# Kernel optimization log

Hardware: AMD Instinct MI355X
Metric: run time of the kernel (lower is better)

The kernel has to match this reference:

```python
import jax, jax.numpy as jnp
import numpy as np
from jax.ops import segment_sum

EPS = 1e-5
N, E = 100000, 1600000
CIN, H, COUT, ED = 32, 64, 16, 16


def _lin(k, fan_in, fan_out):
    return jax.random.normal(k, (fan_in, fan_out), jnp.float32) / np.sqrt(fan_in)


def setup_inputs() -> dict:
    key = jax.random.key(0)
    ks = jax.random.split(key, 24)
    inp = {
        "x": jax.random.normal(ks[0], (N, CIN), jnp.float32),
        "edge_index": jax.random.randint(ks[1], (2, E), 0, N, jnp.int32),
        "edge_attr": jax.random.normal(ks[2], (E, ED), jnp.float32),
    }
    # layer 1 (SAGEConvWithEdgeAttr: in=CIN -> H)
    inp.update(
        l1_Wl=_lin(ks[3], CIN, H), l1_bl=jnp.zeros((H,), jnp.float32),
        l1_Wr=_lin(ks[4], CIN, H),
        l1_We=_lin(ks[5], ED, H), l1_be=jnp.zeros((H,), jnp.float32),
        l1_Wg=_lin(ks[6], 2 * H, H), l1_bg=jnp.zeros((H,), jnp.float32),
        l1_bng=jnp.ones((H,), jnp.float32), l1_bnb=jnp.zeros((H,), jnp.float32),
    )
    # layer 2 (H -> H)
    inp.update(
        l2_Wl=_lin(ks[7], H, H), l2_bl=jnp.zeros((H,), jnp.float32),
        l2_Wr=_lin(ks[8], H, H),
        l2_We=_lin(ks[9], ED, H), l2_be=jnp.zeros((H,), jnp.float32),
        l2_Wg=_lin(ks[10], 2 * H, H), l2_bg=jnp.zeros((H,), jnp.float32),
        l2_bng=jnp.ones((H,), jnp.float32), l2_bnb=jnp.zeros((H,), jnp.float32),
    )
    # GraphNorms (weight=1, bias=0, mean_scale=1 at init; randomize slightly via ones)
    inp.update(
        gn1_g=jnp.ones((H,), jnp.float32), gn1_b=jnp.zeros((H,), jnp.float32), gn1_a=jnp.ones((H,), jnp.float32),
        gn2_g=jnp.ones((H,), jnp.float32), gn2_b=jnp.zeros((H,), jnp.float32), gn2_a=jnp.ones((H,), jnp.float32),
        lin_W=_lin(ks[11], H, COUT), lin_b=jnp.zeros((COUT,), jnp.float32),
    )
    return inp


def _sage_edge_layer(x, row, col, ea, Wl, bl, Wr, We, be, Wg, bg, bng, bnb):
    n = x.shape[0]
    ea_t = ea @ We + be                                        # [E', H]
    deg = segment_sum(jnp.ones_like(col, dtype=x.dtype), col, num_segments=n)
    agg = segment_sum(x[row], col, num_segments=n) / jnp.maximum(deg, 1.0)[:, None]
    out = agg @ Wl + bl + x @ Wr                               # SAGEConv (mean)
    gate = jax.nn.sigmoid(jnp.concatenate([out[col], ea_t], -1) @ Wg + bg)
    out = out + segment_sum(gate * ea_t, col, num_segments=n)  # edge contributions
    mu = out.mean(0)
    var = ((out - mu) ** 2).mean(0)                            # BatchNorm1d (batch stats)
    out = bng * (out - mu) * jax.lax.rsqrt(var + EPS) + bnb
    return jax.nn.relu(2.0 * out)                              # Identity residual + out, relu


def _graph_norm(x, g, b, a):
    mu = x.mean(0)
    xc = x - a * mu
    var = (xc ** 2).mean(0)
    return g * xc * jax.lax.rsqrt(var + EPS) + b


def reference(x, edge_index, edge_attr,
              l1_Wl, l1_bl, l1_Wr, l1_We, l1_be, l1_Wg, l1_bg, l1_bng, l1_bnb,
              l2_Wl, l2_bl, l2_Wr, l2_We, l2_be, l2_Wg, l2_bg, l2_bng, l2_bnb,
              gn1_g, gn1_b, gn1_a, gn2_g, gn2_b, gn2_a, lin_W, lin_b):
    n = x.shape[0]
    loop = jnp.arange(n, dtype=edge_index.dtype)
    row = jnp.concatenate([edge_index[0], loop])               # add_self_loops
    col = jnp.concatenate([edge_index[1], loop])
    ea = jnp.concatenate([edge_attr, jnp.ones((n, edge_attr.shape[1]), edge_attr.dtype)], 0)
    h = _sage_edge_layer(x, row, col, ea, l1_Wl, l1_bl, l1_Wr, l1_We, l1_be, l1_Wg, l1_bg, l1_bng, l1_bnb)
    h = jax.nn.relu(h)
    h = jax.nn.relu(_graph_norm(h, gn1_g, gn1_b, gn1_a))
    h = _sage_edge_layer(h, row, col, ea, l2_Wl, l2_bl, l2_Wr, l2_We, l2_be, l2_Wg, l2_bg, l2_bng, l2_bnb)
    h = jax.nn.relu(h)
    h = jax.nn.relu(_graph_norm(h, gn2_g, gn2_b, gn2_a))
    return h @ lin_W + lin_b
```

## Files before the change

kernel.cpp:

```cpp
#include <hip/hip_runtime.h>
#include <hip/hip_fp16.h>
#include <math.h>
#include <stdint.h>

#define H 64
#define ED 16
#define CO 16
#define WGRID 2048
#define NWAVES (WGRID * 4)
#define CPART 2048
static constexpr float EPSV = 1e-5f;
static constexpr float LOG2E = 1.44269504f;

typedef _Float16 h2v __attribute__((ext_vector_type(2)));
typedef _Float16 f16x8 __attribute__((ext_vector_type(8)));
typedef float f32x4 __attribute__((ext_vector_type(4)));

__device__ __forceinline__ float sigm2(float z) {
    return __builtin_amdgcn_rcpf(1.0f + __builtin_amdgcn_exp2f(-z));
}

__device__ __forceinline__ h2v as_h2(int x) { union { int i; h2v h; } u; u.i = x; return u.h; }

__device__ __forceinline__ f16x8 as_f16x8(int4 v) { union { int4 i; f16x8 h; } u; u.i = v; return u.h; }

__device__ __forceinline__ int pack2(float a, float b) {
    __half2 h = __floats2half2_rn(a, b);
    return *reinterpret_cast<int*>(&h);
}

__global__ void k_prep(const float* __restrict__ We1, const float* __restrict__ be1, const float* __restrict__ Wg1,
                       const float* __restrict__ We2, const float* __restrict__ be2, const float* __restrict__ Wg2,
                       float* __restrict__ ws) {
    int j = threadIdx.x;
    for (int l = 0; l < 2; ++l) {
        const float* We = l ? We2 : We1;
        const float* be = l ? be2 : be1;
        const float* Wg = l ? Wg2 : Wg1;
        int* wth = (int*)(ws + (l ? 1024 : 0));
        int* wgh = (int*)(ws + (l ? 1536 : 512));
        float* ets = ws + 2048 + l * 192;
        float* vs  = ws + 2112 + l * 192;
        float* dv  = ws + 2176 + l * 192;
        float wt[ED], wg[ED];
        float et = be[j];
        for (int k = 0; k < ED; ++k) { wt[k] = We[k * H + j]; et += wt[k]; }
        ets[j] = et;
        float d = 0.f;
        for (int m = 0; m < H; ++m) d += be[m] * Wg[(H + m) * H + j];
        float vsum = d;
        for (int k = 0; k < ED; ++k) {
            float acc = 0.f;
            for (int m = 0; m < H; ++m) acc += We[k * H + m] * Wg[(H + m) * H + j];
            wg[k] = acc;
            vsum += acc;
        }
        dv[j] = d * LOG2E;
        vs[j] = vsum * LOG2E;
        for (int q = 0; q < 8; ++q) {
            wth[j * 8 + q] = pack2(wt[2 * q], wt[2 * q + 1]);
            wgh[j * 8 + q] = pack2(wg[2 * q] * LOG2E, wg[2 * q + 1] * LOG2E);
        }
    }
    for (int s = 0; s < 8; ++s) ws[2432 + s * 64 + j] = 0.f;
}

__global__ void k_xh(const float* __restrict__ x, __half* __restrict__ xh, int total4) {
    int i = blockIdx.x * blockDim.x + threadIdx.x;
    if (i >= total4) return;
    float4 v = *reinterpret_cast<const float4*>(x + (size_t)i * 4);
    __half2 h0 = __floats2half2_rn(v.x, v.y), h1 = __floats2half2_rn(v.z, v.w);
    uint2 o;
    o.x = *reinterpret_cast<unsigned*>(&h0);
    o.y = *reinterpret_cast<unsigned*>(&h1);
    *reinterpret_cast<uint2*>(xh + (size_t)i * 4) = o;
}

__global__ void k_eah(const float* __restrict__ ea, int4* __restrict__ eah, int E) {
    int e = blockIdx.x * blockDim.x + threadIdx.x;
    if (e >= E) return;
    const float4* src = reinterpret_cast<const float4*>(ea + (size_t)e * ED);
    float4 v0 = src[0], v1 = src[1], v2 = src[2], v3 = src[3];
    int hh[8];
    hh[0] = pack2(v0.x, v0.y); hh[1] = pack2(v0.z, v0.w);
    hh[2] = pack2(v1.x, v1.y); hh[3] = pack2(v1.z, v1.w);
    hh[4] = pack2(v2.x, v2.y); hh[5] = pack2(v2.z, v2.w);
    hh[6] = pack2(v3.x, v3.y); hh[7] = pack2(v3.z, v3.w);
    const int4* o = reinterpret_cast<const int4*>(hh);
    eah[(size_t)e * 2 + 0] = o[0];
    eah[(size_t)e * 2 + 1] = o[1];
}

__global__ void k_count(const int* __restrict__ cols, int* __restrict__ cnt, int E) {
    int e = blockIdx.x * blockDim.x + threadIdx.x;
    if (e < E) atomicAdd(&cnt[cols[e]], 1);
}

__global__ __launch_bounds__(1024) void k_scan1(const int* __restrict__ cnt, int* __restrict__ bs, int N) {
    __shared__ int ls[1024];
    int t = threadIdx.x;
    int i = blockIdx.x * 1024 + t;
    ls[t] = (i < N) ? cnt[i] : 0;
    __syncthreads();
    for (int off = 512; off > 0; off >>= 1) {
        if (t < off) ls[t] += ls[t + off];
        __syncthreads();
    }
    if (t == 0) bs[blockIdx.x] = ls[0];
}

__global__ __launch_bounds__(1024) void k_scan2(int* __restrict__ bs, int SB) {
    __shared__ int ls[1024];
    int t = threadIdx.x;
    int v = (t < SB) ? bs[t] : 0;
    ls[t] = v;
    __syncthreads();
    for (int off = 1; off < 1024; off <<= 1) {
        int x = (t >= off) ? ls[t - off] : 0;
        __syncthreads();
        ls[t] += x;
        __syncthreads();
    }
    if (t < SB) bs[t] = ls[t] - v;
}

__global__ __launch_bounds__(1024) void k_scan3(const int* __restrict__ cnt, const int* __restrict__ bs,
                                                int* __restrict__ rowptr, int N, int E) {
    __shared__ int ls[1024];
    int t = threadIdx.x;
    int i = blockIdx.x * 1024 + t;
    int v = (i < N) ? cnt[i] : 0;
    ls[t] = v;
    __syncthreads();
    for (int off = 1; off < 1024; off <<= 1) {
        int x = (t >= off) ? ls[t - off] : 0;
        __syncthreads();
        ls[t] += x;
        __syncthreads();
    }
    if (i < N) rowptr[i] = bs[blockIdx.x] + ls[t] - v;
    if (i == 0) rowptr[N] = E;
}

__global__ void k_ranges(const int* __restrict__ rowptr, int* __restrict__ ranges, int N, int E, int nw) {
    int w = blockIdx.x * blockDim.x + threadIdx.x;
    if (w > nw) return;
    if (w == nw) { ranges[nw] = N; return; }
    int t0 = (int)((long)E * w / nw);
    int lo = 0, hi = N;
    while (lo < hi) { int mid = (lo + hi) >> 1; if (rowptr[mid] < t0) lo = mid + 1; else hi = mid; }
    ranges[w] = lo;
}

__global__ __launch_bounds__(256) void k_part(const int* __restrict__ rows, const int* __restrict__ cols,
                                              int2* __restrict__ tmp, int* __restrict__ offtab,
                                              int E, int NB, int SH) {
    __shared__ int hist[1025];
    __shared__ int pscan[256];
    __shared__ int2 stage[CPART];
    int tid = threadIdx.x;
    int base = blockIdx.x * CPART;
    int cnt = min(CPART, E - base);
    for (int i = tid; i <= NB; i += 256) hist[i] = 0;
    __syncthreads();
    int myc[8], myr[8];
#pragma unroll
    for (int q = 0; q < 8; ++q) {
        int li = q * 256 + tid;
        if (li < cnt) {
            int e = base + li;
            myc[q] = cols[e];
            myr[q] = rows[e];
            atomicAdd(&hist[myc[q] >> SH], 1);
        } else myc[q] = -1;
    }
    __syncthreads();
    int h[4], s = 0;
    int b0 = tid * 4;
#pragma unroll
    for (int k = 0; k < 4; ++k) { h[k] = (b0 + k < NB) ? hist[b0 + k] : 0; s += h[k]; }
    pscan[tid] = s;
    __syncthreads();
    for (int off = 1; off < 256; off <<= 1) {
        int v = (tid >= off) ? pscan[tid - off] : 0;
        __syncthreads();
        pscan[tid] += v;
        __syncthreads();
    }
    int excl = pscan[tid] - s;
    __syncthreads();
    int run = excl;
#pragma unroll
    for (int k = 0; k < 4; ++k) {
        if (b0 + k < NB) hist[b0 + k] = run;
        run += h[k];
    }
    __syncthreads();
    int* ot = offtab + (size_t)blockIdx.x * (NB + 1);
    for (int i = tid; i < NB; i += 256) ot[i] = hist[i];
    if (tid == 0) ot[NB] = cnt;
    __syncthreads();
    int mask = (1 << SH) - 1;
#pragma unroll
    for (int q = 0; q < 8; ++q) {
        if (myc[q] >= 0) {
            int b = myc[q] >> SH;
            int p = atomicAdd(&hist[b], 1);
            int e = base + q * 256 + tid;
            stage[p] = make_int2(myr[q], (e << SH) | (myc[q] & mask));
        }
    }
    __syncthreads();
    int2* dst = tmp + base;
    for (int i = tid; i < cnt; i += 256) dst[i] = stage[i];
}

__global__ __launch_bounds__(1024) void k_build(const int* __restrict__ rowptr, const int2* __restrict__ tmp,
                                               const int* __restrict__ offtab, const int4* __restrict__ eah,
                                               int* __restrict__ erow, __half* __restrict__ eap,
                                               int N, int NB, int SH, int PB) {
    __shared__ int lcur[1024];
    int tid = threadIdx.x;
    int b = blockIdx.x;
    int NPB = 1 << SH;
    int nodelo = b << SH;
    for (int j = tid; j < NPB; j += 1024) {
        int n = nodelo + j;
        lcur[j] = (n < N) ? rowptr[n] : 0;
    }
    __syncthreads();
    int mask = NPB - 1;
    for (int i = tid; i < PB; i += 1024) {
        const int* ot = offtab + (size_t)i * (NB + 1);
        int j0 = ot[b], j1 = ot[b + 1];
        for (int j = j0; j < j1; ++j) {
            int2 v = tmp[(size_t)i * CPART + j];
            int e = (int)(((unsigned)v.y) >> SH);
            int cl = v.y & mask;
            int p = atomicAdd(&lcur[cl], 1);
            erow[p] = v.x;
            int4 a0 = eah[(size_t)e * 2 + 0];
            int4 a1 = eah[(size_t)e * 2 + 1];
            int4* d = reinterpret_cast<int4*>(eap + (size_t)p * ED);
            d[0] = a0; d[1] = a1;
        }
    }
}

template <int CIN, bool GN>
__global__ __launch_bounds__(256) void k_gather(const __half* __restrict__ x, const int* __restrict__ rowptr,
                         const int* __restrict__ ranges,
                         const int* __restrict__ erow, float* __restrict__ agg,
                         const float* __restrict__ s1, const float* __restrict__ s2,
                         const float* __restrict__ gng, const float* __restrict__ gnb,
                         const float* __restrict__ gna, float Ninv, int N) {
    int lane = threadIdx.x & 63;
    int w = (blockIdx.x * blockDim.x + threadIdx.x) >> 6;
    float A = 1.f, B = 0.f;
    if (GN) {
        float mu = s1[lane] * Ninv, m2 = s2[lane] * Ninv, a = gna[lane];
        float var = m2 - 2.f * a * mu * mu + a * a * mu * mu;
        A = gng[lane] * rsqrtf(var + EPSV);
        B = gnb[lane] - A * a * mu;
    }
    int n0 = ranges[w], n1 = ranges[w + 1];
    for (int n = n0; n < n1; ++n) {
        int s = rowptr[n], te = rowptr[n + 1];
        if (CIN == 64) {
            float raw = __half2float(x[(size_t)n * 64 + lane]);
            float acc = GN ? fmaxf(fmaf(A, raw, B), 0.f) : raw;
            int i = s;
            for (; i + 7 < te; i += 8) {
                int r0 = erow[i],     r1 = erow[i + 1], r2 = erow[i + 2], r3 = erow[i + 3];
                int r4 = erow[i + 4], r5 = erow[i + 5], r6 = erow[i + 6], r7 = erow[i + 7];
                float x0 = __half2float(x[(size_t)r0 * 64 + lane]);
                float x1 = __half2float(x[(size_t)r1 * 64 + lane]);
                float x2 = __half2float(x[(size_t)r2 * 64 + lane]);
                float x3 = __half2float(x[(size_t)r3 * 64 + lane]);
                float x4 = __half2float(x[(size_t)r4 * 64 + lane]);
                float x5 = __half2float(x[(size_t)r5 * 64 + lane]);
                float x6 = __half2float(x[(size_t)r6 * 64 + lane]);
                float x7 = __half2float(x[(size_t)r7 * 64 + lane]);
                if (GN) {
                    x0 = fmaxf(fmaf(A, x0, B), 0.f); x1 = fmaxf(fmaf(A, x1, B), 0.f);
                    x2 = fmaxf(fmaf(A, x2, B), 0.f); x3 = fmaxf(fmaf(A, x3, B), 0.f);
                    x4 = fmaxf(fmaf(A, x4, B), 0.f); x5 = fmaxf(fmaf(A, x5, B), 0.f);
                    x6 = fmaxf(fmaf(A, x6, B), 0.f); x7 = fmaxf(fmaf(A, x7, B), 0.f);
                }
                acc += ((x0 + x1) + (x2 + x3)) + ((x4 + x5) + (x6 + x7));
            }
            for (; i < te; ++i) {
                float xv = __half2float(x[(size_t)erow[i] * 64 + lane]);
                if (GN) xv = fmaxf(fmaf(A, xv, B), 0.f);
                acc += xv;
            }
            agg[(size_t)n * H + lane] = acc;
        } else {
            int c = lane & 31, half = lane >> 5;
            float acc = half ? 0.f : __half2float(x[(size_t)n * 32 + c]);
            int i = s + half;
            for (; i + 6 < te; i += 8) {
                int r0 = erow[i], r1 = erow[i + 2], r2 = erow[i + 4], r3 = erow[i + 6];
                float x0 = __half2float(x[(size_t)r0 * 32 + c]);
                float x1 = __half2float(x[(size_t)r1 * 32 + c]);
                float x2 = __half2float(x[(size_t)r2 * 32 + c]);
                float x3 = __half2float(x[(size_t)r3 * 32 + c]);
                acc += (x0 + x1) + (x2 + x3);
            }
            for (; i < te; i += 2) acc += __half2float(x[(size_t)erow[i] * 32 + c]);
            acc += __shfl_xor(acc, 32);
            if (half == 0) agg[(size_t)n * H + c] = acc;
        }
    }
}

#define MT4A(mq, aval) \
    acc[mq][0] = fmaf(aval, w1.x, acc[mq][0]); acc[mq][1] = fmaf(aval, w1.y, acc[mq][1]); \
    acc[mq][2] = fmaf(aval, w1.z, acc[mq][2]); acc[mq][3] = fmaf(aval, w1.w, acc[mq][3]);
#define MT4X(mq, aval) \
    acc[mq][0] = fmaf(aval, w2.x, acc[mq][0]); acc[mq][1] = fmaf(aval, w2.y, acc[mq][1]); \
    acc[mq][2] = fmaf(aval, w2.z, acc[mq][2]); acc[mq][3] = fmaf(aval, w2.w, acc[mq][3]);

template <int K, bool GN>
__global__ __launch_bounds__(256) void k_gemmfu(
        const float* __restrict__ A,
        const __half* __restrict__ A2, int lda2,
        const float* __restrict__ W1, const float* __restrict__ W2,
        const float* __restrict__ bias,
        const float* __restrict__ Wg, const float* __restrict__ bg,
        const float* __restrict__ s1, const float* __restrict__ s2,
        const float* __restrict__ gng, const float* __restrict__ gnb,
        const float* __restrict__ gna, float Ninv,
        const int* __restrict__ rowptr,
        __half* __restrict__ pre, __half* __restrict__ uout, int N) {
    __shared__ float WA[64 * 64];
    __shared__ float WB[K * 64];
    __shared__ float big[64][68];
    __shared__ float As[64], Bs[64], invd[64];
    int tid = threadIdx.x;
    for (int idx = tid; idx < K * 64; idx += 256) { WA[idx] = W1[idx]; WB[idx] = W2[idx]; }
    int nb = blockIdx.x * 64;
    if (tid < 64) {
        if (GN) {
            float mu = s1[tid] * Ninv, m2 = s2[tid] * Ninv, a = gna[tid];
            float var = m2 - 2.f * a * mu * mu + a * a * mu * mu;
            float Av = gng[tid] * rsqrtf(var + EPSV);
            As[tid] = Av; Bs[tid] = gnb[tid] - Av * a * mu;
        }
        int n = nb + tid;
        invd[tid] = (n < N) ? 1.f / (float)(rowptr[n + 1] - rowptr[n] + 1) : 0.f;
    }
    __syncthreads();
    int tm = tid >> 4, tn = tid & 15;
    int m0 = tm * 4, j0 = tn * 4;
    float acc[4][4];
#pragma unroll
    for (int jq = 0; jq < 4; ++jq) {
        float b = bias[j0 + jq];
#pragma unroll
        for (int mq = 0; mq < 4; ++mq) acc[mq][jq] = b;
    }
    int sn = tid >> 2, kq4 = (tid & 3) * 4;
    int sg = nb + sn;
    for (int k0 = 0; k0 < K; k0 += 16) {
        if (k0) __syncthreads();
        if (sg < N) {
            float4 av = *reinterpret_cast<const float4*>(A + (size_t)sg * 64 + k0 + kq4);
            float sc = invd[sn];
            av.x *= sc; av.y *= sc; av.z *= sc; av.w *= sc;
            big[kq4 + 0][sn] = av.x; big[kq4 + 1][sn] = av.y;
            big[kq4 + 2][sn] = av.z; big[kq4 + 3][sn] = av.w;
            uint2 hv = *reinterpret_cast<const uint2*>(A2 + (size_t)sg * lda2 + k0 + kq4);
            __half2 h01 = *reinterpret_cast<__half2*>(&hv.x);
            __half2 h23 = *reinterpret_cast<__half2*>(&hv.y);
            float2 f01 = __half22float2(h01), f23 = __half22float2(h23);
            float xv0 = f01.x, xv1 = f01.y, xv2 = f23.x, xv3 = f23.y;
            if (GN) {
                xv0 = fmaxf(fmaf(As[k0 + kq4 + 0], xv0, Bs[k0 + kq4 + 0]), 0.f);
                xv1 = fmaxf(fmaf(As[k0 + kq4 + 1], xv1, Bs[k0 + kq4 + 1]), 0.f);
                xv2 = fmaxf(fmaf(As[k0 + kq4 + 2], xv2, Bs[k0 + kq4 + 2]), 0.f);
                xv3 = fmaxf(fmaf(As[k0 + kq4 + 3], xv3, Bs[k0 + kq4 + 3]), 0.f);
            }
            big[16 + kq4 + 0][sn] = xv0; big[16 + kq4 + 1][sn] = xv1;
            big[16 + kq4 + 2][sn] = xv2; big[16 + kq4 + 3][sn] = xv3;
        } else {
#pragma unroll
            for (int q = 0; q < 4; ++q) { big[kq4 + q][sn] = 0.f; big[16 + kq4 + q][sn] = 0.f; }
        }
        __syncthreads();
#pragma unroll
        for (int k = 0; k < 16; ++k) {
            float4 am = *reinterpret_cast<const float4*>(&big[k][m0]);
            float4 w1 = *reinterpret_cast<const float4*>(&WA[(k0 + k) * 64 + j0]);
            MT4A(0, am.x) MT4A(1, am.y) MT4A(2, am.z) MT4A(3, am.w)
            float4 xm = *reinterpret_cast<const float4*>(&big[16 + k][m0]);
            float4 w2 = *reinterpret_cast<const float4*>(&WB[(k0 + k) * 64 + j0]);
            MT4X(0, xm.x) MT4X(1, xm.y) MT4X(2, xm.z) MT4X(3, xm.w)
        }
    }
    __syncthreads();
#pragma unroll
    for (int mq = 0; mq < 4; ++mq) {
        int n = nb + m0 + mq;
        if (n < N) {
            uint2 o;
            o.x = pack2(acc[mq][0], acc[mq][1]);
            o.y = pack2(acc[mq][2], acc[mq][3]);
            *reinterpret_cast<uint2*>(pre + (size_t)n * 64 + j0) = o;
        }
#pragma unroll
        for (int jq = 0; jq < 4; ++jq) big[j0 + jq][m0 + mq] = acc[mq][jq];
    }
    for (int idx = tid; idx < 4096; idx += 256) WA[idx] = Wg[idx] * LOG2E;
    __syncthreads();
    float acc2[4][4];
#pragma unroll
    for (int jq = 0; jq < 4; ++jq) {
        float b = bg[j0 + jq] * LOG2E;
#pragma unroll
        for (int mq = 0; mq < 4; ++mq) acc2[mq][jq] = b;
    }
#pragma unroll 8
    for (int k = 0; k < 64; ++k) {
        float4 pm = *reinterpret_cast<const float4*>(&big[k][m0]);
        float4 w1 = *reinterpret_cast<const float4*>(&WA[k * 64 + j0]);
        acc2[0][0] = fmaf(pm.x, w1.x, acc2[0][0]); acc2[0][1] = fmaf(pm.x, w1.y, acc2[0][1]);
        acc2[0][2] = fmaf(pm.x, w1.z, acc2[0][2]); acc2[0][3] = fmaf(pm.x, w1.w, acc2[0][3]);
        acc2[1][0] = fmaf(pm.y, w1.x, acc2[1][0]); acc2[1][1] = fmaf(pm.y, w1.y, acc2[1][1]);
        acc2[1][2] = fmaf(pm.y, w1.z, acc2[1][2]); acc2[1][3] = fmaf(pm.y, w1.w, acc2[1][3]);
        acc2[2][0] = fmaf(pm.z, w1.x, acc2[2][0]); acc2[2][1] = fmaf(pm.z, w1.y, acc2[2][1]);
        acc2[2][2] = fmaf(pm.z, w1.z, acc2[2][2]); acc2[2][3] = fmaf(pm.z, w1.w, acc2[2][3]);
        acc2[3][0] = fmaf(pm.w, w1.x, acc2[3][0]); acc2[3][1] = fmaf(pm.w, w1.y, acc2[3][1]);
        acc2[3][2] = fmaf(pm.w, w1.z, acc2[3][2]); acc2[3][3] = fmaf(pm.w, w1.w, acc2[3][3]);
    }
#pragma unroll
    for (int mq = 0; mq < 4; ++mq) {
        int n = nb + m0 + mq;
        if (n < N) {
            uint2 o;
            o.x = pack2(acc2[mq][0], acc2[mq][1]);
            o.y = pack2(acc2[mq][2], acc2[mq][3]);
            *reinterpret_cast<uint2*>(uout + (size_t)n * 64 + j0) = o;
        }
    }
}

__global__ __launch_bounds__(256) void k_gate(
        const int* __restrict__ rowptr, const int* __restrict__ ranges,
        const __half* __restrict__ eap,
        const int* __restrict__ wth, const int* __restrict__ wgh,
        const float* __restrict__ be, const float* __restrict__ dv,
        const float* __restrict__ ets, const float* __restrict__ vs,
        const __half* __restrict__ u, __half* __restrict__ pre,
        float* __restrict__ s1, float* __restrict__ s2, int N) {
    __shared__ __align__(16) int4 estage[4][128];
    __shared__ unsigned pvet[4][16][68];
    __shared__ float ls[2][4][H];
    int lane = threadIdx.x & 63;
    int wv = threadIdx.x >> 6;
    int w = (blockIdx.x << 2) | wv;
    int g = lane >> 4, li = lane & 15;
    f16x8 Bet[4], Bv[4];
#pragma unroll
    for (int c = 0; c < 4; ++c) {
        int j = c * 16 + li;
        int4 bt = make_int4(0, 0, 0, 0), bv = make_int4(0, 0, 0, 0);
        if (g < 2) {
            bt = *reinterpret_cast<const int4*>(&wth[j * 8 + g * 4]);
            bv = *reinterpret_cast<const int4*>(&wgh[j * 8 + g * 4]);
        }
        Bet[c] = as_f16x8(bt);
        Bv[c] = as_f16x8(bv);
        if (g == 2) {
            Bet[c][0] = (_Float16)be[j];
            Bv[c][0]  = (_Float16)dv[j];
        }
    }
    float ets_l = ets[lane], vs_l = vs[lane];
    int n0 = ranges[w], n1 = ranges[w + 1];
    float s = 0.f, ss = 0.f;
    if (n0 < n1) {
        int4* dst = &estage[wv][0];
        const int4* gsrc = reinterpret_cast<const int4*>(eap);
        int e0 = rowptr[n0], e1 = rowptr[n1];
        int n = n0;
        int nend = rowptr[n0 + 1];
        size_t idx = (size_t)n * H + lane;
        float u_l = __half2float(u[idx]);
        float pv = __half2float(pre[idx]);
        int np = min(n + 1, n1 - 1);
        size_t idxn = (size_t)np * H + lane;
        float u_n = __half2float(u[idxn]);
        float pv_n = __half2float(pre[idxn]);
        float acc = sigm2(u_l + vs_l) * ets_l;
        {
            int bytes = min(64, e1 - e0) * 32;
            int4 p0, p1;
            if (lane * 16 < bytes) p0 = gsrc[(size_t)e0 * 2 + lane];
            if (1024 + lane * 16 < bytes) p1 = gsrc[(size_t)e0 * 2 + 64 + lane];
            if (lane * 16 < bytes) dst[lane] = p0;
            if (1024 + lane * 16 < bytes) dst[64 + lane] = p1;
        }
        for (int c = e0; c < e1; c += 64) {
            int cnt = min(64, e1 - c);
            int nbytes = (c + 64 < e1) ? min(64, e1 - c - 64) * 32 : 0;
            int4 p0, p1;
            if (lane * 16 < nbytes) p0 = gsrc[(size_t)(c + 64) * 2 + lane];
            if (1024 + lane * 16 < nbytes) p1 = gsrc[(size_t)(c + 64) * 2 + 64 + lane];
            for (int tb = 0; tb < cnt; tb += 16) {
                int4 af = make_int4(0, 0, 0, 0);
                if (g < 2) af = dst[(tb + li) * 2 + g];
                f16x8 Af = as_f16x8(af);
                if (g == 2) Af[0] = (_Float16)1.0f;
                f32x4 z = {0.f, 0.f, 0.f, 0.f};
                f32x4 et0 = __builtin_amdgcn_mfma_f32_16x16x32_f16(Af, Bet[0], z, 0, 0, 0);
                f32x4 et1 = __builtin_amdgcn_mfma_f32_16x16x32_f16(Af, Bet[1], z, 0, 0, 0);
                f32x4 et2 = __builtin_amdgcn_mfma_f32_16x16x32_f16(Af, Bet[2], z, 0, 0, 0);
                f32x4 et3 = __builtin_amdgcn_mfma_f32_16x16x32_f16(Af, Bet[3], z, 0, 0, 0);
                f32x4 vv0 = __builtin_amdgcn_mfma_f32_16x16x32_f16(Af, Bv[0], z, 0, 0, 0);
                f32x4 vv1 = __builtin_amdgcn_mfma_f32_16x16x32_f16(Af, Bv[1], z, 0, 0, 0);
                f32x4 vv2 = __builtin_amdgcn_mfma_f32_16x16x32_f16(Af, Bv[2], z, 0, 0, 0);
                f32x4 vv3 = __builtin_amdgcn_mfma_f32_16x16x32_f16(Af, Bv[3], z, 0, 0, 0);
                int r0 = g * 4;
#pragma unroll
                for (int r = 0; r < 4; ++r) {
                    pvet[wv][r0 + r][li]      = (unsigned)pack2(vv0[r], et0[r]);
                    pvet[wv][r0 + r][16 + li] = (unsigned)pack2(vv1[r], et1[r]);
                    pvet[wv][r0 + r][32 + li] = (unsigned)pack2(vv2[r], et2[r]);
                    pvet[wv][r0 + r][48 + li] = (unsigned)pack2(vv3[r], et3[r]);
                }
                int p = tb, pend = min(cnt, tb + 16);
                while (p < pend) {
                    while (c + p == nend) {
                        float tval = pv + acc;
                        pre[idx] = __float2half(tval);
                        s += tval; ss += tval * tval;
                        ++n;
                        idx = idxn; u_l = u_n; pv = pv_n;
                        np = min(n + 1, n1 - 1);
                        idxn = (size_t)np * H + lane;
                        u_n = __half2float(u[idxn]);
                        pv_n = __half2float(pre[idxn]);
                        acc = sigm2(u_l + vs_l) * ets_l;
                        nend = rowptr[n + 1];
                    }
                    int lim = min(pend, nend - c);
                    for (; p + 1 < lim; p += 2) {
                        unsigned w0 = pvet[wv][p - tb][lane];
                        unsigned w1 = pvet[wv][p + 1 - tb][lane];
                        float2 f0 = __half22float2(*reinterpret_cast<__half2*>(&w0));
                        float2 f1 = __half22float2(*reinterpret_cast<__half2*>(&w1));
                        acc += sigm2(u_l + f0.x) * f0.y + sigm2(u_l + f1.x) * f1.y;
                    }
                    if (p < lim) {
                        unsigned w0 = pvet[wv][p - tb][lane];
                        float2 f0 = __half22float2(*reinterpret_cast<__half2*>(&w0));
                        acc += sigm2(u_l + f0.x) * f0.y;
                        ++p;
                    }
                }
            }
            if (lane * 16 < nbytes) dst[lane] = p0;
            if (1024 + lane * 16 < nbytes) dst[64 + lane] = p1;
        }
        for (;;) {
            float tval = pv + acc;
            pre[idx] = __float2half(tval);
            s += tval; ss += tval * tval;
            ++n;
            if (n >= n1) break;
            idx = idxn; u_l = u_n; pv = pv_n;
            np = min(n + 1, n1 - 1);
            idxn = (size_t)np * H + lane;
            u_n = __half2float(u[idxn]);
            pv_n = __half2float(pre[idxn]);
            acc = sigm2(u_l + vs_l) * ets_l;
        }
    }
    ls[0][wv][lane] = s; ls[1][wv][lane] = ss;
    __syncthreads();
    if (threadIdx.x < H) {
        float a = ls[0][0][lane] + ls[0][1][lane] + ls[0][2][lane] + ls[0][3][lane];
        float b = ls[1][0][lane] + ls[1][1][lane] + ls[1][2][lane] + ls[1][3][lane];
        atomicAdd(&s1[lane], a);
        atomicAdd(&s2[lane], b);
    }
}

__global__ void k_apply(const __half* __restrict__ in, __half* __restrict__ outb,
                        const float* __restrict__ bng, const float* __restrict__ bnb,
                        const float* __restrict__ s1b, const float* __restrict__ s2b,
                        float* __restrict__ s1g, float* __restrict__ s2g, float Ninv, int N) {
    int j = threadIdx.x, ty = threadIdx.y;
    __shared__ float As[H], Bs[H];
    if (ty == 0) {
        float mu = s1b[j] * Ninv, var = s2b[j] * Ninv - mu * mu;
        float r = rsqrtf(var + EPSV);
        float A = 2.f * bng[j] * r;
        As[j] = A; Bs[j] = 2.f * (bnb[j] - bng[j] * r * mu);
    }
    __syncthreads();
    float A = As[j], B = Bs[j];
    float s = 0.f, ss = 0.f;
    for (int n = blockIdx.x * 4 + ty; n < N; n += gridDim.x * 4) {
        size_t idx = (size_t)n * H + j;
        float v = fmaxf(fmaf(A, __half2float(in[idx]), B), 0.f);
        outb[idx] = __float2half(v);
        s += v; ss += v * v;
    }
    __shared__ float ls[2][4][H];
    ls[0][ty][j] = s; ls[1][ty][j] = ss;
    __syncthreads();
    if (ty == 0) {
        float a = ls[0][0][j] + ls[0][1][j] + ls[0][2][j] + ls[0][3][j];
        float b = ls[1][0][j] + ls[1][1][j] + ls[1][2][j] + ls[1][3][j];
        atomicAdd(&s1g[j], a);
        atomicAdd(&s2g[j], b);
    }
}

__global__ __launch_bounds__(256) void k_final(const __half* __restrict__ hraw, const float* __restrict__ W,
                        const float* __restrict__ bias,
                        const float* __restrict__ s1, const float* __restrict__ s2,
                        const float* __restrict__ gng, const float* __restrict__ gnb,
                        const float* __restrict__ gna, float Ninv,
                        float* __restrict__ outp, int N) {
    __shared__ float As[H], Bs[H];
    if (threadIdx.x < H) {
        int j = threadIdx.x;
        float mu = s1[j] * Ninv, m2 = s2[j] * Ninv, a = gna[j];
        float var = m2 - 2.f * a * mu * mu + a * a * mu * mu;
        float A = gng[j] * rsqrtf(var + EPSV);
        As[j] = A; Bs[j] = gnb[j] - A * a * mu;
    }
    __syncthreads();
    int n = blockIdx.x * blockDim.x + threadIdx.x;
    if (n >= N) return;
    float o[CO];
#pragma unroll
    for (int t = 0; t < CO; ++t) o[t] = bias[t];
    const __half* hr = hraw + (size_t)n * H;
    for (int m4 = 0; m4 < H / 4; ++m4) {
        uint2 hv = *reinterpret_cast<const uint2*>(hr + m4 * 4);
        __half2 h01 = *reinterpret_cast<__half2*>(&hv.x);
        __half2 h23 = *reinterpret_cast<__half2*>(&hv.y);
        float2 f01 = __half22float2(h01), f23 = __half22float2(h23);
        float hx = fmaxf(fmaf(As[m4*4+0], f01.x, Bs[m4*4+0]), 0.f);
        float hy = fmaxf(fmaf(As[m4*4+1], f01.y, Bs[m4*4+1]), 0.f);
        float hz = fmaxf(fmaf(As[m4*4+2], f23.x, Bs[m4*4+2]), 0.f);
        float hw = fmaxf(fmaf(As[m4*4+3], f23.y, Bs[m4*4+3]), 0.f);
#pragma unroll
        for (int t = 0; t < CO; ++t) {
            o[t] += hx * W[(m4*4+0) * CO + t];
            o[t] += hy * W[(m4*4+1) * CO + t];
            o[t] += hz * W[(m4*4+2) * CO + t];
            o[t] += hw * W[(m4*4+3) * CO + t];
        }
    }
    float* orow = outp + (size_t)n * CO;
#pragma unroll
    for (int t4 = 0; t4 < CO / 4; ++t4)
        reinterpret_cast<float4*>(orow)[t4] = make_float4(o[t4*4+0], o[t4*4+1], o[t4*4+2], o[t4*4+3]);
}

extern "C" void kernel_launch(void* const* d_in, const int* in_sizes, int n_in,
                              void* d_out, int out_size, void* d_ws, size_t ws_size,
                              hipStream_t stream) {
    const float* x     = (const float*)d_in[0];
    const int*   ei    = (const int*)d_in[1];
    const float* ea    = (const float*)d_in[2];
    const float* l1_Wl = (const float*)d_in[3];  const float* l1_bl = (const float*)d_in[4];
    const float* l1_Wr = (const float*)d_in[5];  const float* l1_We = (const float*)d_in[6];
    const float* l1_be = (const float*)d_in[7];  const float* l1_Wg = (const float*)d_in[8];
    const float* l1_bg = (const float*)d_in[9];  const float* l1_bng= (const float*)d_in[10];
    const float* l1_bnb= (const float*)d_in[11];
    const float* l2_Wl = (const float*)d_in[12]; const float* l2_bl = (const float*)d_in[13];
    const float* l2_Wr = (const float*)d_in[14]; const float* l2_We = (const float*)d_in[15];
    const float* l2_be = (const float*)d_in[16]; const float* l2_Wg = (const float*)d_in[17];
    const float* l2_bg = (const float*)d_in[18]; const float* l2_bng= (const float*)d_in[19];
    const float* l2_bnb= (const float*)d_in[20];
    const float* gn1_g = (const float*)d_in[21]; const float* gn1_b = (const float*)d_in[22];
    const float* gn1_a = (const float*)d_in[23];
    const float* gn2_g = (const float*)d_in[24]; const float* gn2_b = (const float*)d_in[25];
    const float* gn2_a = (const float*)d_in[26];
    const float* lin_W = (const float*)d_in[27]; const float* lin_b = (const float*)d_in[28];

    const int N = in_sizes[0] / 32;
    const int E = in_sizes[1] / 2;
    const int* rows = ei;
    const int* cols = ei + E;

    int SH = 7, NPB = 128;
    while (((N + NPB - 1) >> SH) > 1024) { SH++; NPB <<= 1; }
    const int NB = (N + NPB - 1) >> SH;
    const int PB = (E + CPART - 1) / CPART;

    float* w    = (float*)d_ws;
    int* wth1   = (int*)w;
    int* wgh1   = (int*)(w + 512);
    int* wth2   = (int*)(w + 1024);
    int* wgh2   = (int*)(w + 1536);
    float* ets1 = w + 2048; float* vs1 = w + 2112; float* dv1 = w + 2176;
    float* ets2 = w + 2240; float* vs2 = w + 2304; float* dv2 = w + 2368;
    float* stats= w + 2432;

    int* ip     = (int*)(w + 8192);
    int* rowptr = ip;
    int* cnt    = ip + (N + 1);
    int* bs     = cnt + N;
    int* ranges = bs + 1024;
    int* erow   = ranges + (NWAVES + 2);

    uintptr_t pa = (uintptr_t)(erow + E);
    pa = (pa + 255) & ~(uintptr_t)255;
    __half* eap = (__half*)pa;
    uintptr_t px = (uintptr_t)(eap + (size_t)E * ED);
    px = (px + 255) & ~(uintptr_t)255;
    __half* xh = (__half*)px;
    uintptr_t pz = (uintptr_t)(xh + (size_t)N * 32);
    pz = (pz + 255) & ~(uintptr_t)255;

    int2* tmp   = (int2*)pz;
    int* offtab = (int*)(tmp + E);
    uintptr_t pe = (uintptr_t)(offtab + (size_t)PB * (NB + 1));
    pe = (pe + 255) & ~(uintptr_t)255;
    int4* eah = (int4*)pe;

    size_t NB64 = (size_t)N * H;
    float* B0 = (float*)pz;
    __half* Bpre = (__half*)(B0 + NB64);
    __half* Bu   = Bpre + NB64;
    __half* B3h  = Bu + NB64;
    __half* B0h  = (__half*)B0;

    const float Ninv = 1.0f / (float)N;
    dim3 rb(64, 4);
    int egrid = (E + 255) / 256;
    int ngrid = (N + 255) / 256;
    int g64 = (N + 63) / 64;
    const int SB = (N + 1023) >> 10;

    k_prep<<<1, 64, 0, stream>>>(l1_We, l1_be, l1_Wg, l2_We, l2_be, l2_Wg, w);
    k_xh<<<(N * 8 + 255) / 256, 256, 0, stream>>>(x, xh, N * 8);
    k_eah<<<egrid, 256, 0, stream>>>(ea, eah, E);

    hipMemsetAsync(cnt, 0, sizeof(int) * (size_t)N, stream);
    k_count<<<egrid, 256, 0, stream>>>(cols, cnt, E);
    k_scan1<<<SB, 1024, 0, stream>>>(cnt, bs, N);
    k_scan2<<<1, 1024, 0, stream>>>(bs, SB);
    k_scan3<<<SB, 1024, 0, stream>>>(cnt, bs, rowptr, N, E);
    k_ranges<<<(NWAVES + 256) / 256, 256, 0, stream>>>(rowptr, ranges, N, E, NWAVES);
    k_part<<<PB, 256, 0, stream>>>(rows, cols, tmp, offtab, E, NB, SH);
    k_build<<<NB, 1024, 0, stream>>>(rowptr, tmp, offtab, eah, erow, eap, N, NB, SH, PB);

    k_gather<32, false><<<WGRID, 256, 0, stream>>>(xh, rowptr, ranges, erow, B0,
                                                   nullptr, nullptr, nullptr, nullptr, nullptr, 0.f, N);
    k_gemmfu<32, false><<<g64, 256, 0, stream>>>(B0, xh, 32, l1_Wl, l1_Wr, l1_bl, l1_Wg, l1_bg,
                                                 nullptr, nullptr, nullptr, nullptr, nullptr, 0.f,
                                                 rowptr, Bpre, Bu, N);
    k_gate<<<WGRID, 256, 0, stream>>>(rowptr, ranges, eap, wth1, wgh1, l1_be, dv1, ets1, vs1,
                                      Bu, Bpre, stats + 0, stats + 64, N);
    k_apply<<<256, rb, 0, stream>>>(Bpre, B3h, l1_bng, l1_bnb, stats + 0, stats + 64,
                                    stats + 128, stats + 192, Ninv, N);

    k_gather<64, true><<<WGRID, 256, 0, stream>>>(B3h, rowptr, ranges, erow, B0,
                                                  stats + 128, stats + 192, gn1_g, gn1_b, gn1_a, Ninv, N);
    k_gemmfu<64, true><<<g64, 256, 0, stream>>>(B0, B3h, 64, l2_Wl, l2_Wr, l2_bl, l2_Wg, l2_bg,
                                                stats + 128, stats + 192, gn1_g, gn1_b, gn1_a, Ninv,
                                                rowptr, Bpre, Bu, N);
    k_gate<<<WGRID, 256, 0, stream>>>(rowptr, ranges, eap, wth2, wgh2, l2_be, dv2, ets2, vs2,
                                      Bu, Bpre, stats + 256, stats + 320, N);
    k_apply<<<256, rb, 0, stream>>>(Bpre, B0h, l2_bng, l2_bnb, stats + 256, stats + 320,
                                    stats + 384, stats + 448, Ninv, N);

    k_final<<<ngrid, 256, 0, stream>>>(B0h, lin_W, lin_b, stats + 384, stats + 448,
                                       gn2_g, gn2_b, gn2_a, Ninv, (float*)d_out, N);
}
```

Before: 676.5 us.

## Fuse edge-attr fp16 conversion into partition pass and carry payload through buckets

Removes the separate k_eah kernel and has k_part convert each edge's attributes to fp16 and stage them alongside the key in shared memory, writing them bucket-ordered into a temp payload buffer. k_build then reads the payload contiguously instead of gathering eah by edge id, which removes a random 32-byte read per edge and the edge id packed into the key. CPART is halved to 1024 so the larger shared staging (key plus 32-byte payload) fits, which doubles the number of partition blocks and the size of the offset table. The temp buffer layout changes, so tmpk/tmpp/offtab must still fit inside the B0 aliasing region.

Measured after the change: 674.0 us. No clear change (-0.4%).

```diff
diff --git a/kernel.cpp b/kernel.cpp
--- a/kernel.cpp
+++ b/kernel.cpp
@@ -8,7 +8,7 @@
 #define CO 16
 #define WGRID 2048
 #define NWAVES (WGRID * 4)
-#define CPART 2048
+#define CPART 1024
 static constexpr float EPSV = 1e-5f;
 static constexpr float LOG2E = 1.44269504f;
 
@@ -76,21 +76,6 @@
     *reinterpret_cast<uint2*>(xh + (size_t)i * 4) = o;
 }
 
-__global__ void k_eah(const float* __restrict__ ea, int4* __restrict__ eah, int E) {
-    int e = blockIdx.x * blockDim.x + threadIdx.x;
-    if (e >= E) return;
-    const float4* src = reinterpret_cast<const float4*>(ea + (size_t)e * ED);
-    float4 v0 = src[0], v1 = src[1], v2 = src[2], v3 = src[3];
-    int hh[8];
-    hh[0] = pack2(v0.x, v0.y); hh[1] = pack2(v0.z, v0.w);
-    hh[2] = pack2(v1.x, v1.y); hh[3] = pack2(v1.z, v1.w);
-    hh[4] = pack2(v2.x, v2.y); hh[5] = pack2(v2.z, v2.w);
-    hh[6] = pack2(v3.x, v3.y); hh[7] = pack2(v3.z, v3.w);
-    const int4* o = reinterpret_cast<const int4*>(hh);
-    eah[(size_t)e * 2 + 0] = o[0];
-    eah[(size_t)e * 2 + 1] = o[1];
-}
-
 __global__ void k_count(const int* __restrict__ cols, int* __restrict__ cnt, int E) {
     int e = blockIdx.x * blockDim.x + threadIdx.x;
     if (e < E) atomicAdd(&cnt[cols[e]], 1);
@@ -153,24 +138,37 @@
 }
 
 __global__ __launch_bounds__(256) void k_part(const int* __restrict__ rows, const int* __restrict__ cols,
-                                              int2* __restrict__ tmp, int* __restrict__ offtab,
+                                              const float* __restrict__ ea,
+                                              int2* __restrict__ tmpk, int4* __restrict__ tmpp,
+                                              int* __restrict__ offtab,
                                               int E, int NB, int SH) {
     __shared__ int hist[1025];
     __shared__ int pscan[256];
-    __shared__ int2 stage[CPART];
+    __shared__ int2 skey[CPART];
+    __shared__ int4 spay[CPART][2];
     int tid = threadIdx.x;
     int base = blockIdx.x * CPART;
     int cnt = min(CPART, E - base);
     for (int i = tid; i <= NB; i += 256) hist[i] = 0;
     __syncthreads();
-    int myc[8], myr[8];
-#pragma unroll
-    for (int q = 0; q < 8; ++q) {
+    int myc[4], myr[4];
+    int4 pa0[4], pa1[4];
+#pragma unroll
+    for (int q = 0; q < 4; ++q) {
         int li = q * 256 + tid;
         if (li < cnt) {
             int e = base + li;
             myc[q] = cols[e];
             myr[q] = rows[e];
+            const float4* src = reinterpret_cast<const float4*>(ea + (size_t)e * ED);
+            float4 v0 = src[0], v1 = src[1], v2 = src[2], v3 = src[3];
+            int hh[8];
+            hh[0] = pack2(v0.x, v0.y); hh[1] = pack2(v0.z, v0.w);
+            hh[2] = pack2(v1.x, v1.y); hh[3] = pack2(v1.z, v1.w);
+            hh[4] = pack2(v2.x, v2.y); hh[5] = pack2(v2.z, v2.w);
+            hh[6] = pack2(v3.x, v3.y); hh[7] = pack2(v3.z, v3.w);
+            pa0[q] = reinterpret_cast<const int4*>(hh)[0];
+            pa1[q] = reinterpret_cast<const int4*>(hh)[1];
             atomicAdd(&hist[myc[q] >> SH], 1);
         } else myc[q] = -1;
     }
@@ -202,21 +200,26 @@
     __syncthreads();
     int mask = (1 << SH) - 1;
 #pragma unroll
-    for (int q = 0; q < 8; ++q) {
+    for (int q = 0; q < 4; ++q) {
         if (myc[q] >= 0) {
             int b = myc[q] >> SH;
             int p = atomicAdd(&hist[b], 1);
-            int e = base + q * 256 + tid;
-            stage[p] = make_int2(myr[q], (e << SH) | (myc[q] & mask));
-        }
-    }
-    __syncthreads();
-    int2* dst = tmp + base;
-    for (int i = tid; i < cnt; i += 256) dst[i] = stage[i];
-}
-
-__global__ __launch_bounds__(1024) void k_build(const int* __restrict__ rowptr, const int2* __restrict__ tmp,
-                                               const int* __restrict__ offtab, const int4* __restrict__ eah,
+            skey[p] = make_int2(myr[q], myc[q] & mask);
+            spay[p][0] = pa0[q];
+            spay[p][1] = pa1[q];
+        }
+    }
+    __syncthreads();
+    for (int i = tid; i < cnt; i += 256) {
+        tmpk[base + i] = skey[i];
+        tmpp[(size_t)(base + i) * 2 + 0] = spay[i][0];
+        tmpp[(size_t)(base + i) * 2 + 1] = spay[i][1];
+    }
+}
+
+__global__ __launch_bounds__(1024) void k_build(const int* __restrict__ rowptr, const int2* __restrict__ tmpk,
+                                               const int4* __restrict__ tmpp,
+                                               const int* __restrict__ offtab,
                                                int* __restrict__ erow, __half* __restrict__ eap,
                                                int N, int NB, int SH, int PB) {
     __shared__ int lcur[1024];
@@ -229,18 +232,16 @@
         lcur[j] = (n < N) ? rowptr[n] : 0;
     }
     __syncthreads();
-    int mask = NPB - 1;
     for (int i = tid; i < PB; i += 1024) {
         const int* ot = offtab + (size_t)i * (NB + 1);
         int j0 = ot[b], j1 = ot[b + 1];
         for (int j = j0; j < j1; ++j) {
-            int2 v = tmp[(size_t)i * CPART + j];
-            int e = (int)(((unsigned)v.y) >> SH);
-            int cl = v.y & mask;
-            int p = atomicAdd(&lcur[cl], 1);
-            erow[p] = v.x;
-            int4 a0 = eah[(size_t)e * 2 + 0];
-            int4 a1 = eah[(size_t)e * 2 + 1];
+            size_t src = (size_t)i * CPART + j;
+            int2 k = tmpk[src];
+            int4 a0 = tmpp[src * 2 + 0];
+            int4 a1 = tmpp[src * 2 + 1];
+            int p = atomicAdd(&lcur[k.y], 1);
+            erow[p] = k.x;
             int4* d = reinterpret_cast<int4*>(eap + (size_t)p * ED);
             d[0] = a0; d[1] = a1;
         }
@@ -720,11 +721,9 @@
     uintptr_t pz = (uintptr_t)(xh + (size_t)N * 32);
     pz = (pz + 255) & ~(uintptr_t)255;
 
-    int2* tmp   = (int2*)pz;
-    int* offtab = (int*)(tmp + E);
-    uintptr_t pe = (uintptr_t)(offtab + (size_t)PB * (NB + 1));
-    pe = (pe + 255) & ~(uintptr_t)255;
-    int4* eah = (int4*)pe;
+    int2* tmpk  = (int2*)pz;
+    int4* tmpp  = (int4*)(tmpk + E);
+    int* offtab = (int*)(tmpp + (size_t)E * 2);
 
     size_t NB64 = (size_t)N * H;
     float* B0 = (float*)pz;
@@ -742,7 +741,6 @@
 
     k_prep<<<1, 64, 0, stream>>>(l1_We, l1_be, l1_Wg, l2_We, l2_be, l2_Wg, w);
     k_xh<<<(N * 8 + 255) / 256, 256, 0, stream>>>(x, xh, N * 8);
-    k_eah<<<egrid, 256, 0, stream>>>(ea, eah, E);
 
     hipMemsetAsync(cnt, 0, sizeof(int) * (size_t)N, stream);
     k_count<<<egrid, 256, 0, stream>>>(cols, cnt, E);
@@ -750,8 +748,8 @@
     k_scan2<<<1, 1024, 0, stream>>>(bs, SB);
     k_scan3<<<SB, 1024, 0, stream>>>(cnt, bs, rowptr, N, E);
     k_ranges<<<(NWAVES + 256) / 256, 256, 0, stream>>>(rowptr, ranges, N, E, NWAVES);
-    k_part<<<PB, 256, 0, stream>>>(rows, cols, tmp, offtab, E, NB, SH);
-    k_build<<<NB, 1024, 0, stream>>>(rowptr, tmp, offtab, eah, erow, eap, N, NB, SH, PB);
+    k_part<<<PB, 256, 0, stream>>>(rows, cols, ea, tmpk, tmpp, offtab, E, NB, SH);
+    k_build<<<NB, 1024, 0, stream>>>(rowptr, tmpk, tmpp, offtab, erow, eap, N, NB, SH, PB);
 
     k_gather<32, false><<<WGRID, 256, 0, stream>>>(xh, rowptr, ranges, erow, B0,
                                                    nullptr, nullptr, nullptr, nullptr, nullptr, 0.f, N);
```
